# Kernel tuning notes

Hardware: AMD Instinct MI355X
Metric: run time of the kernel (lower is better)

The kernel has to match this reference:

```python
import jax, jax.numpy as jnp
import numpy as np
from functools import partial

H = 1024  # hidden_sz
B, T = 32, 256
NL = 4    # stacked LSTM layers
WSCALE = 0.02


def setup_inputs() -> dict:
    key = jax.random.key(0)
    ks = jax.random.split(key, 8)
    x = jax.random.normal(ks[0], (B, T, H), dtype=jnp.float32)
    h0 = jnp.zeros((B, H), dtype=jnp.float32)
    c0 = jnp.zeros((B, H), dtype=jnp.float32)
    # LSTM params per layer: kernel [H,4H], recurrent kernel [H,4H], bias [4H]
    Wk = jax.random.normal(ks[1], (NL, H, 4 * H), dtype=jnp.float32) * WSCALE
    Wr = jax.random.normal(ks[2], (NL, H, 4 * H), dtype=jnp.float32) * WSCALE
    b = jnp.zeros((NL, 4 * H), dtype=jnp.float32)
    # dense head
    Wd = jax.random.normal(ks[3], (H, H), dtype=jnp.float32) * WSCALE
    bd = jnp.zeros((H,), dtype=jnp.float32)
    return {"x": x, "h0": h0, "c0": c0, "Wk": Wk, "Wr": Wr, "b": b, "Wd": Wd, "bd": bd}


def _lstm_layer(x_tbd, h0, c0, Wk, Wr, b):
    # Keras LSTM with activation='relu', recurrent_activation='sigmoid'.
    # Gate order in keras kernels: i, f, c(candidate), o.
    xw = jnp.einsum('tbd,dg->tbg', x_tbd, Wk) + b  # precompute input projections [T,B,4H]

    def step(carry, xw_t):
        h, c = carry
        z = xw_t + h @ Wr  # [B,4H]
        i, f, g, o = jnp.split(z, 4, axis=-1)
        i = jax.nn.sigmoid(i)
        f = jax.nn.sigmoid(f)
        o = jax.nn.sigmoid(o)
        c = f * c + i * jax.nn.relu(g)
        h = o * jax.nn.relu(c)
        return (h, c), h

    (hT, cT), hs = jax.lax.scan(step, (h0, c0), xw)
    return hs, hT, cT  # hs: [T,B,H]


def reference(x, h0, c0, Wk, Wr, b, Wd, bd):
    # x: [B,T,H] -> time-major [T,B,H]
    seq = jnp.transpose(x, (1, 0, 2))
    h, c = h0, c0
    for l in range(NL):
        seq, h, c = _lstm_layer(seq, h, c, Wk[l], Wr[l], b[l])
        # dropout layers are identity at inference (training=False)
    out = jnp.einsum('tbh,hd->tbd', seq, Wd) + bd
    out = jnp.transpose(out, (1, 0, 2))  # back to [B,T,H]
    return out, h, c
```

## Files before the change

### kernel.cpp

```cpp
#include <hip/hip_runtime.h>

#define TT 256
#define BB 32
#define HH 1024
#define GG 4096

typedef __attribute__((ext_vector_type(8))) short short8;
typedef __attribute__((ext_vector_type(4))) float f32x4;

__device__ __forceinline__ unsigned short rne_bf16(float x) {
    unsigned u = __float_as_uint(x);
    unsigned r = (u + 0x7FFFu + ((u >> 16) & 1u)) >> 16;
    return (unsigned short)r;
}
__device__ __forceinline__ float bf16f(unsigned short s) {
    return __uint_as_float((unsigned)s << 16);
}

__global__ __launch_bounds__(256) void k_transpose3(const float* __restrict__ x,
                                                    unsigned short* __restrict__ s1,
                                                    unsigned short* __restrict__ s2,
                                                    unsigned short* __restrict__ s3) {
    int idx = blockIdx.x * 256 + threadIdx.x;
    int k4 = idx & 255;
    int tb = idx >> 8;
    int t = tb >> 5, b = tb & 31;
    float4 v = ((const float4*)x)[((size_t)b * TT + t) * 256 + k4];
    float xs[4] = {v.x, v.y, v.z, v.w};
    ushort4 o1, o2, o3;
    unsigned short* p1 = (unsigned short*)&o1;
    unsigned short* p2 = (unsigned short*)&o2;
    unsigned short* p3 = (unsigned short*)&o3;
#pragma unroll
    for (int e = 0; e < 4; ++e) {
        unsigned short q1 = rne_bf16(xs[e]);
        float r1 = xs[e] - bf16f(q1);
        unsigned short q2 = rne_bf16(r1);
        float r2 = r1 - bf16f(q2);
        p1[e] = q1; p2[e] = q2; p3[e] = rne_bf16(r2);
    }
    size_t off = (size_t)tb * HH + k4 * 4;
    *(ushort4*)&s1[off] = o1;
    *(ushort4*)&s2[off] = o2;
    *(ushort4*)&s3[off] = o3;
}

__global__ __launch_bounds__(256) void k_transpose(const float* __restrict__ x, float* __restrict__ seq) {
    int idx = blockIdx.x * 256 + threadIdx.x;
    int k4 = idx & 255;
    int tb = idx >> 8;
    int t = tb >> 5, b = tb & 31;
    float4 v = ((const float4*)x)[((size_t)b * TT + t) * 256 + k4];
    ((float4*)seq)[(size_t)tb * 256 + k4] = v;
}

__global__ __launch_bounds__(256) void k_init_hc(const float* __restrict__ h0, const float* __restrict__ c0,
                                                 float* __restrict__ h, float* __restrict__ c) {
    int i = blockIdx.x * 256 + threadIdx.x;
    ((float4*)h)[i] = ((const float4*)h0)[i];
    ((float4*)c)[i] = ((const float4*)c0)[i];
}

__global__ __launch_bounds__(256) void k_init_hc2(const float* __restrict__ h0, const float* __restrict__ c0,
                                                  float* __restrict__ h, float* __restrict__ c,
                                                  unsigned short* __restrict__ hb1,
                                                  unsigned short* __restrict__ hb2,
                                                  unsigned short* __restrict__ hb3) {
    int i = blockIdx.x * 256 + threadIdx.x;
    float4 hv = ((const float4*)h0)[i];
    ((float4*)h)[i] = hv;
    ((float4*)c)[i] = ((const float4*)c0)[i];
    float xs[4] = {hv.x, hv.y, hv.z, hv.w};
    ushort4 o1, o2, o3;
    unsigned short* p1 = (unsigned short*)&o1;
    unsigned short* p2 = (unsigned short*)&o2;
    unsigned short* p3 = (unsigned short*)&o3;
#pragma unroll
    for (int e = 0; e < 4; ++e) {
        unsigned short s1 = rne_bf16(xs[e]);
        float r1 = xs[e] - bf16f(s1);
        unsigned short s2 = rne_bf16(r1);
        float r2 = r1 - bf16f(s2);
        p1[e] = s1; p2[e] = s2; p3[e] = rne_bf16(r2);
    }
    *(ushort4*)&hb1[i * 4] = o1;
    *(ushort4*)&hb2[i * 4] = o2;
    *(ushort4*)&hb3[i * 4] = o3;
}

__global__ __launch_bounds__(256) void k_copy_hc(const float* __restrict__ h, const float* __restrict__ c,
                                                 float* __restrict__ oh, float* __restrict__ oc) {
    int i = blockIdx.x * 256 + threadIdx.x;
    ((float4*)oh)[i] = ((const float4*)h)[i];
    ((float4*)oc)[i] = ((const float4*)c)[i];
}

__global__ __launch_bounds__(256) void k_wrt(const float* __restrict__ Wr, float* __restrict__ WrT) {
    __shared__ float tile[64][65];
    int c0 = blockIdx.x * 64;
    int k0 = blockIdx.y * 64;
    int tid = threadIdx.x;
    int tr = tid >> 4, tc4 = tid & 15;
#pragma unroll
    for (int p = 0; p < 4; ++p) {
        int r = p * 16 + tr;
        float4 v = *(const float4*)&Wr[(size_t)(k0 + r) * GG + c0 + tc4 * 4];
        tile[r][tc4 * 4 + 0] = v.x;
        tile[r][tc4 * 4 + 1] = v.y;
        tile[r][tc4 * 4 + 2] = v.z;
        tile[r][tc4 * 4 + 3] = v.w;
    }
    __syncthreads();
#pragma unroll
    for (int p = 0; p < 4; ++p) {
        int cc = p * 16 + tr;
        float4 v;
        v.x = tile[tc4 * 4 + 0][cc];
        v.y = tile[tc4 * 4 + 1][cc];
        v.z = tile[tc4 * 4 + 2][cc];
        v.w = tile[tc4 * 4 + 3][cc];
        *(float4*)&WrT[(size_t)(c0 + cc) * 1024 + k0 + tc4 * 4] = v;
    }
}

__global__ __launch_bounds__(256) void k_wrt3(const float* __restrict__ Wr, unsigned short* __restrict__ W1,
                                              unsigned short* __restrict__ W2, unsigned short* __restrict__ W3) {
    __shared__ float tile[64][65];
    int c0 = blockIdx.x * 64;
    int k0 = blockIdx.y * 64;
    int tid = threadIdx.x;
    int tr = tid >> 4, tc4 = tid & 15;
#pragma unroll
    for (int p = 0; p < 4; ++p) {
        int r = p * 16 + tr;
        float4 v = *(const float4*)&Wr[(size_t)(k0 + r) * GG + c0 + tc4 * 4];
        tile[r][tc4 * 4 + 0] = v.x;
        tile[r][tc4 * 4 + 1] = v.y;
        tile[r][tc4 * 4 + 2] = v.z;
        tile[r][tc4 * 4 + 3] = v.w;
    }
    __syncthreads();
    int cc = tid & 63, kq = tid >> 6;
    int G = c0 + cc;
    int outrow = ((G & 1023) >> 2) * 16 + (G >> 10) * 4 + (G & 3);
    size_t obase = (size_t)outrow * 1024 + k0 + kq * 16;
    unsigned short t1[16], t2[16], t3[16];
#pragma unroll
    for (int e = 0; e < 16; ++e) {
        float v = tile[kq * 16 + e][cc];
        unsigned short s1 = rne_bf16(v);
        float r1 = v - bf16f(s1);
        unsigned short s2 = rne_bf16(r1);
        float r2 = r1 - bf16f(s2);
        t1[e] = s1; t2[e] = s2; t3[e] = rne_bf16(r2);
    }
#pragma unroll
    for (int hlf = 0; hlf < 2; ++hlf) {
        *(short8*)&W1[obase + hlf * 8] = *(short8*)&t1[hlf * 8];
        *(short8*)&W2[obase + hlf * 8] = *(short8*)&t2[hlf * 8];
        *(short8*)&W3[obase + hlf * 8] = *(short8*)&t3[hlf * 8];
    }
}

__global__ __launch_bounds__(256) void k_wt3(const float* __restrict__ W, int N,
                                             unsigned short* __restrict__ W1,
                                             unsigned short* __restrict__ W2,
                                             unsigned short* __restrict__ W3) {
    __shared__ float tile[64][65];
    int c0 = blockIdx.x * 64;
    int k0 = blockIdx.y * 64;
    int tid = threadIdx.x;
    int tr = tid >> 4, tc4 = tid & 15;
#pragma unroll
    for (int p = 0; p < 4; ++p) {
        int r = p * 16 + tr;
        float4 v = *(const float4*)&W[(size_t)(k0 + r) * N + c0 + tc4 * 4];
        tile[r][tc4 * 4 + 0] = v.x;
        tile[r][tc4 * 4 + 1] = v.y;
        tile[r][tc4 * 4 + 2] = v.z;
        tile[r][tc4 * 4 + 3] = v.w;
    }
    __syncthreads();
#pragma unroll
    for (int p = 0; p < 4; ++p) {
        int cc = p * 16 + tr;
        ushort4 o1, o2, o3;
        unsigned short* po1 = (unsigned short*)&o1;
        unsigned short* po2 = (unsigned short*)&o2;
        unsigned short* po3 = (unsigned short*)&o3;
#pragma unroll
        for (int e = 0; e < 4; ++e) {
            float v = tile[tc4 * 4 + e][cc];
            unsigned short s1 = rne_bf16(v);
            float r1 = v - bf16f(s1);
            unsigned short s2 = rne_bf16(r1);
            float r2 = r1 - bf16f(s2);
            po1[e] = s1; po2[e] = s2; po3[e] = rne_bf16(r2);
        }
        size_t off = (size_t)(c0 + cc) * 1024 + k0 + tc4 * 4;
        *(ushort4*)&W1[off] = o1;
        *(ushort4*)&W2[off] = o2;
        *(ushort4*)&W3[off] = o3;
    }
}

template <int MODE>
__global__ __launch_bounds__(256, 2) void k_gemm_mx3s(const unsigned short* __restrict__ A1,
                                                      const unsigned short* __restrict__ A2,
                                                      const unsigned short* __restrict__ A3,
                                                      const unsigned short* __restrict__ B1,
                                                      const unsigned short* __restrict__ B2,
                                                      const unsigned short* __restrict__ B3,
                                                      const float* __restrict__ bias, float* __restrict__ C) {
    __shared__ unsigned short Asl[3][6144];
    __shared__ unsigned short Bsl[3][6144];
    int tid = threadIdx.x;
    int m0 = blockIdx.x * 128, n0 = blockIdx.y * 128;
    int lane = tid & 63, wv = tid >> 6;
    int wr = (wv >> 1) * 64, wc = (wv & 1) * 64;
    int l15 = lane & 15, ko = (lane >> 4) * 8;

    f32x4 acc[4][4];
#pragma unroll
    for (int i = 0; i < 4; ++i)
#pragma unroll
        for (int j = 0; j < 4; ++j) acc[i][j] = (f32x4){0.f, 0.f, 0.f, 0.f};

    const unsigned short* Ag[3] = {A1, A2, A3};
    const unsigned short* Bg[3] = {B1, B2, B3};

    for (int k0 = 0; k0 < 1024; k0 += 32) {
#pragma unroll
        for (int sp = 0; sp < 3; ++sp) {
#pragma unroll
            for (int i = 0; i < 2; ++i) {
                int idx = i * 256 + tid;
                int r = idx >> 2, kq = idx & 3;
                short8 va = *(const short8*)&Ag[sp][(size_t)(m0 + r) * 1024 + k0 + kq * 8];
                *(short8*)&Asl[sp][r * 48 + kq * 8] = va;
                short8 vb = *(const short8*)&Bg[sp][(size_t)(n0 + r) * 1024 + k0 + kq * 8];
                *(short8*)&Bsl[sp][r * 48 + kq * 8] = vb;
            }
        }
        __syncthreads();

        short8 af[3][4];
#pragma unroll
        for (int mi = 0; mi < 4; ++mi) {
            int ro = (wr + mi * 16 + l15) * 48 + ko;
#pragma unroll
            for (int sp = 0; sp < 3; ++sp) af[sp][mi] = *(const short8*)&Asl[sp][ro];
        }
#pragma unroll
        for (int ni = 0; ni < 4; ++ni) {
            int co = (wc + ni * 16 + l15) * 48 + ko;
            short8 b0 = *(const short8*)&Bsl[0][co];
            short8 b1 = *(const short8*)&Bsl[1][co];
            short8 b2 = *(const short8*)&Bsl[2][co];
#pragma unroll
            for (int mi = 0; mi < 4; ++mi) {
                f32x4 a = acc[mi][ni];
                a = __builtin_amdgcn_mfma_f32_16x16x32_bf16(af[0][mi], b0, a, 0, 0, 0);
                a = __builtin_amdgcn_mfma_f32_16x16x32_bf16(af[1][mi], b0, a, 0, 0, 0);
                a = __builtin_amdgcn_mfma_f32_16x16x32_bf16(af[0][mi], b1, a, 0, 0, 0);
                a = __builtin_amdgcn_mfma_f32_16x16x32_bf16(af[2][mi], b0, a, 0, 0, 0);
                a = __builtin_amdgcn_mfma_f32_16x16x32_bf16(af[1][mi], b1, a, 0, 0, 0);
                a = __builtin_amdgcn_mfma_f32_16x16x32_bf16(af[0][mi], b2, a, 0, 0, 0);
                acc[mi][ni] = a;
            }
        }
        __syncthreads();
    }

#pragma unroll
    for (int ni = 0; ni < 4; ++ni) {
        int col = n0 + wc + ni * 16 + l15;
        float bv = bias[col];
#pragma unroll
        for (int mi = 0; mi < 4; ++mi) {
            int rbase = m0 + wr + mi * 16 + (lane >> 4) * 4;
#pragma unroll
            for (int r = 0; r < 4; ++r) {
                int m = rbase + r;
                if (MODE == 0) {
                    C[(size_t)m * 4096 + col] = acc[mi][ni][r] + bv;
                } else {
                    int t = m >> 5, b = m & 31;
                    C[((size_t)b * TT + t) * HH + col] = acc[mi][ni][r] + bv;
                }
            }
        }
    }
}

__global__ __launch_bounds__(256, 2) void k_gemm_mx3(const float* __restrict__ A,
                                                     const unsigned short* __restrict__ B1,
                                                     const unsigned short* __restrict__ B2,
                                                     const unsigned short* __restrict__ B3,
                                                     const float* __restrict__ bias, float* __restrict__ C) {
    __shared__ unsigned short Asl[3][6144];
    __shared__ unsigned short Bsl[3][6144];
    int tid = threadIdx.x;
    int m0 = blockIdx.x * 128, n0 = blockIdx.y * 128;
    int lane = tid & 63, wv = tid >> 6;
    int wr = (wv >> 1) * 64, wc = (wv & 1) * 64;
    int l15 = lane & 15, ko = (lane >> 4) * 8;

    f32x4 acc[4][4];
#pragma unroll
    for (int i = 0; i < 4; ++i)
#pragma unroll
        for (int j = 0; j < 4; ++j) acc[i][j] = (f32x4){0.f, 0.f, 0.f, 0.f};

    const unsigned short* Bg[3] = {B1, B2, B3};

    for (int k0 = 0; k0 < 1024; k0 += 32) {
#pragma unroll
        for (int i = 0; i < 4; ++i) {
            int idx = i * 256 + tid;
            int m = idx >> 3, kq = idx & 7;
            float4 v = *(const float4*)&A[(size_t)(m0 + m) * 1024 + k0 + kq * 4];
            float xs[4] = {v.x, v.y, v.z, v.w};
            ushort4 o1, o2, o3;
            unsigned short* po1 = (unsigned short*)&o1;
            unsigned short* po2 = (unsigned short*)&o2;
            unsigned short* po3 = (unsigned short*)&o3;
#pragma unroll
            for (int e = 0; e < 4; ++e) {
                unsigned short s1 = rne_bf16(xs[e]);
                float r1 = xs[e] - bf16f(s1);
                unsigned short s2 = rne_bf16(r1);
                float r2 = r1 - bf16f(s2);
                po1[e] = s1; po2[e] = s2; po3[e] = rne_bf16(r2);
            }
            int loff = m * 48 + kq * 4;
            *(ushort4*)&Asl[0][loff] = o1;
            *(ushort4*)&Asl[1][loff] = o2;
            *(ushort4*)&Asl[2][loff] = o3;
        }
#pragma unroll
        for (int sp = 0; sp < 3; ++sp) {
            const unsigned short* bg = Bg[sp];
#pragma unroll
            for (int i = 0; i < 2; ++i) {
                int idx = i * 256 + tid;
                int n = idx >> 2, kq = idx & 3;
                short8 v = *(const short8*)&bg[(size_t)(n0 + n) * 1024 + k0 + kq * 8];
                *(short8*)&Bsl[sp][n * 48 + kq * 8] = v;
            }
        }
        __syncthreads();

        short8 af[3][4];
#pragma unroll
        for (int mi = 0; mi < 4; ++mi) {
            int ro = (wr + mi * 16 + l15) * 48 + ko;
#pragma unroll
            for (int sp = 0; sp < 3; ++sp) af[sp][mi] = *(const short8*)&Asl[sp][ro];
        }
#pragma unroll
        for (int ni = 0; ni < 4; ++ni) {
            int co = (wc + ni * 16 + l15) * 48 + ko;
            short8 b0 = *(const short8*)&Bsl[0][co];
            short8 b1 = *(const short8*)&Bsl[1][co];
            short8 b2 = *(const short8*)&Bsl[2][co];
#pragma unroll
            for (int mi = 0; mi < 4; ++mi) {
                f32x4 a = acc[mi][ni];
                a = __builtin_amdgcn_mfma_f32_16x16x32_bf16(af[0][mi], b0, a, 0, 0, 0);
                a = __builtin_amdgcn_mfma_f32_16x16x32_bf16(af[1][mi], b0, a, 0, 0, 0);
                a = __builtin_amdgcn_mfma_f32_16x16x32_bf16(af[0][mi], b1, a, 0, 0, 0);
                a = __builtin_amdgcn_mfma_f32_16x16x32_bf16(af[2][mi], b0, a, 0, 0, 0);
                a = __builtin_amdgcn_mfma_f32_16x16x32_bf16(af[1][mi], b1, a, 0, 0, 0);
                a = __builtin_amdgcn_mfma_f32_16x16x32_bf16(af[0][mi], b2, a, 0, 0, 0);
                acc[mi][ni] = a;
            }
        }
        __syncthreads();
    }

#pragma unroll
    for (int ni = 0; ni < 4; ++ni) {
        int col = n0 + wc + ni * 16 + l15;
        float bv = bias[col];
#pragma unroll
        for (int mi = 0; mi < 4; ++mi) {
            int rbase = m0 + wr + mi * 16 + (lane >> 4) * 4;
#pragma unroll
            for (int r = 0; r < 4; ++r)
                C[(size_t)(rbase + r) * 4096 + col] = acc[mi][ni][r] + bv;
        }
    }
}

template <int MODE>
__global__ __launch_bounds__(256) void k_gemm(const float* __restrict__ A, const float* __restrict__ W,
                                              const float* __restrict__ bias, float* __restrict__ C, int N) {
    __shared__ float As[16][132];
    __shared__ float Bs[16][132];
    const int K = 1024;
    int tid = threadIdx.x;
    int m0 = blockIdx.x * 128, n0 = blockIdx.y * 128;
    int tx = tid & 15, ty = tid >> 4;
    int a_row = tid >> 2, a_kq = tid & 3;
    int b_cq = tid & 31, b_k = tid >> 5;
    float acc[8][8];
#pragma unroll
    for (int i = 0; i < 8; ++i)
#pragma unroll
        for (int jj = 0; jj < 8; ++jj) acc[i][jj] = 0.f;

    for (int kc = 0; kc < K; kc += 16) {
#pragma unroll
        for (int it = 0; it < 2; ++it) {
            int row = a_row + it * 64;
            float4 v = *(const float4*)&A[(size_t)(m0 + row) * K + kc + a_kq * 4];
            As[a_kq * 4 + 0][row] = v.x;
            As[a_kq * 4 + 1][row] = v.y;
            As[a_kq * 4 + 2][row] = v.z;
            As[a_kq * 4 + 3][row] = v.w;
        }
#pragma unroll
        for (int it = 0; it < 2; ++it) {
            int kk = b_k + it * 8;
            float4 v = *(const float4*)&W[(size_t)(kc + kk) * N + n0 + b_cq * 4];
            *(float4*)&Bs[kk][b_cq * 4] = v;
        }
        __syncthreads();
#pragma unroll
        for (int kk = 0; kk < 16; ++kk) {
            float4 a0 = *(const float4*)&As[kk][ty * 8];
            float4 a1 = *(const float4*)&As[kk][ty * 8 + 4];
            float4 b0 = *(const float4*)&Bs[kk][tx * 8];
            float4 b1 = *(const float4*)&Bs[kk][tx * 8 + 4];
            float am[8] = {a0.x, a0.y, a0.z, a0.w, a1.x, a1.y, a1.z, a1.w};
            float bv[8] = {b0.x, b0.y, b0.z, b0.w, b1.x, b1.y, b1.z, b1.w};
#pragma unroll
            for (int i = 0; i < 8; ++i)
#pragma unroll
                for (int jj = 0; jj < 8; ++jj) acc[i][jj] += am[i] * bv[jj];
        }
        __syncthreads();
    }
#pragma unroll
    for (int i = 0; i < 8; ++i) {
        int m = m0 + ty * 8 + i;
#pragma unroll
        for (int jj = 0; jj < 8; jj += 4) {
            int n = n0 + tx * 8 + jj;
            float4 v;
            v.x = acc[i][jj + 0] + bias[n + 0];
            v.y = acc[i][jj + 1] + bias[n + 1];
            v.z = acc[i][jj + 2] + bias[n + 2];
            v.w = acc[i][jj + 3] + bias[n + 3];
            if (MODE == 0) {
                *(float4*)&C[(size_t)m * N + n] = v;
            } else {
                int t = m >> 5, b = m & 31;
                *(float4*)&C[((size_t)b * TT + t) * HH + n] = v;
            }
        }
    }
}

__global__ __launch_bounds__(512) void k_step_mfma(
    const unsigned short* __restrict__ Wb1, const unsigned short* __restrict__ Wb2,
    const unsigned short* __restrict__ Wb3,
    const unsigned short* __restrict__ Ha1, const unsigned short* __restrict__ Ha2,
    const unsigned short* __restrict__ Ha3,
    unsigned short* __restrict__ Ho1, unsigned short* __restrict__ Ho2,
    unsigned short* __restrict__ Ho3,
    const float* __restrict__ xw_t,
    unsigned short* __restrict__ sq1, unsigned short* __restrict__ sq2,
    unsigned short* __restrict__ sq3, float* __restrict__ seq_t,
    float* __restrict__ h_out, float* __restrict__ c) {
    __shared__ float zs[8][16][33];
    int tid = threadIdx.x;
    int lane = tid & 63, wv = tid >> 6;
    int blk = blockIdx.x;
    int l15 = lane & 15, ko = (lane >> 4) * 8;

    int rb = tid >> 2, rd = tid & 3;
    float pz[4];
    if (tid < 128) {
#pragma unroll
        for (int g = 0; g < 4; ++g) pz[g] = xw_t[rb * GG + g * HH + blk * 4 + rd];
    }

    size_t bbase  = ((size_t)blk * 16 + l15) * 1024 + ko;
    size_t abase0 = (size_t)l15 * 1024 + ko;
    size_t abase1 = (size_t)(16 + l15) * 1024 + ko;

    f32x4 acc0 = (f32x4){0.f, 0.f, 0.f, 0.f};
    f32x4 acc1 = (f32x4){0.f, 0.f, 0.f, 0.f};

#pragma unroll
    for (int kt = 0; kt < 4; ++kt) {
        int kk = (wv * 4 + kt) * 32;
        short8 b0  = *(const short8*)&Wb1[bbase + kk];
        short8 b1  = *(const short8*)&Wb2[bbase + kk];
        short8 b2  = *(const short8*)&Wb3[bbase + kk];
        short8 a00 = *(const short8*)&Ha1[abase0 + kk];
        short8 a01 = *(const short8*)&Ha2[abase0 + kk];
        short8 a02 = *(const short8*)&Ha3[abase0 + kk];
        short8 a10 = *(const short8*)&Ha1[abase1 + kk];
        short8 a11 = *(const short8*)&Ha2[abase1 + kk];
        short8 a12 = *(const short8*)&Ha3[abase1 + kk];
        acc0 = __builtin_amdgcn_mfma_f32_16x16x32_bf16(a00, b0, acc0, 0, 0, 0);
        acc0 = __builtin_amdgcn_mfma_f32_16x16x32_bf16(a01, b0, acc0, 0, 0, 0);
        acc0 = __builtin_amdgcn_mfma_f32_16x16x32_bf16(a00, b1, acc0, 0, 0, 0);
        acc0 = __builtin_amdgcn_mfma_f32_16x16x32_bf16(a02, b0, acc0, 0, 0, 0);
        acc0 = __builtin_amdgcn_mfma_f32_16x16x32_bf16(a01, b1, acc0, 0, 0, 0);
        acc0 = __builtin_amdgcn_mfma_f32_16x16x32_bf16(a00, b2, acc0, 0, 0, 0);
        acc1 = __builtin_amdgcn_mfma_f32_16x16x32_bf16(a10, b0, acc1, 0, 0, 0);
        acc1 = __builtin_amdgcn_mfma_f32_16x16x32_bf16(a11, b0, acc1, 0, 0, 0);
        acc1 = __builtin_amdgcn_mfma_f32_16x16x32_bf16(a10, b1, acc1, 0, 0, 0);
        acc1 = __builtin_amdgcn_mfma_f32_16x16x32_bf16(a12, b0, acc1, 0, 0, 0);
        acc1 = __builtin_amdgcn_mfma_f32_16x16x32_bf16(a11, b1, acc1, 0, 0, 0);
        acc1 = __builtin_amdgcn_mfma_f32_16x16x32_bf16(a10, b2, acc1, 0, 0, 0);
    }

#pragma unroll
    for (int r = 0; r < 4; ++r) {
        zs[wv][l15][(lane >> 4) * 4 + r]      = acc0[r];
        zs[wv][l15][16 + (lane >> 4) * 4 + r] = acc1[r];
    }
    __syncthreads();

    if (tid < 128) {
        float zz[4];
#pragma unroll
        for (int g = 0; g < 4; ++g) {
            float s = pz[g];
#pragma unroll
            for (int u = 0; u < 8; ++u) s += zs[u][g * 4 + rd][rb];
            zz[g] = s;
        }
        float si = 1.f / (1.f + expf(-zz[0]));
        float sf = 1.f / (1.f + expf(-zz[1]));
        float gg = fmaxf(zz[2], 0.f);
        float so = 1.f / (1.f + expf(-zz[3]));
        int hi = rb * HH + blk * 4 + rd;
        float cv = c[hi];
        cv = sf * cv + si * gg;
        c[hi] = cv;
        float hn = so * fmaxf(cv, 0.f);
        h_out[hi] = hn;
        unsigned short s1 = rne_bf16(hn);
        float r1 = hn - bf16f(s1);
        unsigned short s2 = rne_bf16(r1);
        float r2 = r1 - bf16f(s2);
        unsigned short s3 = rne_bf16(r2);
        Ho1[hi] = s1; Ho2[hi] = s2; Ho3[hi] = s3;
        if (sq1) {
            sq1[hi] = s1; sq2[hi] = s2; sq3[hi] = s3;
        } else {
            seq_t[hi] = hn;
        }
    }
}

__global__ __launch_bounds__(512) void k_step_T3(const float* __restrict__ WrT, const float* __restrict__ xw_t,
                                                 float* __restrict__ seq_t, const float* __restrict__ h_in,
                                                 float* __restrict__ h_out, float* __restrict__ c) {
    __shared__ float h_lds[34816];
    __shared__ float zred[8][32][17];
    int tid = threadIdx.x;
    int j = tid & 15, ks = tid >> 4;
    int hc0 = blockIdx.x * 4;
    int col = (j >> 2) * HH + hc0 + (j & 3);

    const float4* WrT4 = (const float4*)WrT;
    int wbase = col * 256 + ks * 8;
    float4 w[8];
#pragma unroll
    for (int q = 0; q < 8; ++q) w[q] = WrT4[wbase + q];

    int rb = tid >> 2, rd = tid & 3;
    float pz[4];
    if (tid < 128) {
#pragma unroll
        for (int g = 0; g < 4; ++g) pz[g] = xw_t[rb * GG + g * HH + hc0 + rd];
    }

    const float4* hp4 = (const float4*)h_in;
    float4* hl4w = (float4*)h_lds;
#pragma unroll 8
    for (int it = 0; it < 16; ++it) {
        int gi = it * 512 + tid;
        float4 v = hp4[gi];
        int b = gi >> 8, kk = gi & 255;
        hl4w[b * 272 + (kk >> 4) * 17 + (kk & 15)] = v;
    }
    __syncthreads();

    const float4* hl4 = (const float4*)h_lds;
    int base4 = (ks >> 1) * 17 + (ks & 1) * 8;
    float acc[32];
#pragma unroll
    for (int b = 0; b < 32; ++b) acc[b] = 0.f;
#pragma unroll
    for (int q = 0; q < 8; ++q) {
        float4 wq = w[q];
#pragma unroll
        for (int b = 0; b < 32; ++b) {
            float4 hv = hl4[b * 272 + base4 + q];
            acc[b] += wq.x * hv.x + wq.y * hv.y + wq.z * hv.z + wq.w * hv.w;
        }
    }
#pragma unroll
    for (int b = 0; b < 32; ++b) {
        acc[b] += __shfl_xor(acc[b], 16);
        acc[b] += __shfl_xor(acc[b], 32);
    }
    int wv = tid >> 6;
    if ((ks & 3) == 0) {
#pragma unroll
        for (int b = 0; b < 32; ++b) zred[wv][b][j] = acc[b];
    }
    __syncthreads();

    if (tid < 128) {
        float zz[4];
#pragma unroll
        for (int g = 0; g < 4; ++g) {
            float s = pz[g];
#pragma unroll
            for (int u = 0; u < 8; ++u) s += zred[u][rb][g * 4 + rd];
            zz[g] = s;
        }
        float si = 1.f / (1.f + expf(-zz[0]));
        float sf = 1.f / (1.f + expf(-zz[1]));
        float gg = fmaxf(zz[2], 0.f);
        float so = 1.f / (1.f + expf(-zz[3]));
        float cv = c[rb * HH + hc0 + rd];
        cv = sf * cv + si * gg;
        c[rb * HH + hc0 + rd] = cv;
        float hn = so * fmaxf(cv, 0.f);
        h_out[rb * HH + hc0 + rd] = hn;
        seq_t[rb * HH + hc0 + rd] = hn;
    }
}

__global__ __launch_bounds__(256) void k_step(const float* __restrict__ Wr, const float* __restrict__ xw_t,
                                              float* __restrict__ seq_t, const float* __restrict__ h_in,
                                              float* __restrict__ h_out, float* __restrict__ c) {
    __shared__ float zred[4][32][17];
    int tid = threadIdx.x;
    int j = tid & 15, ks = tid >> 4;
    int hc0 = blockIdx.x * 4;
    int col = (j >> 2) * HH + hc0 + (j & 3);
    float4 w[16];
#pragma unroll
    for (int q = 0; q < 16; ++q) {
        size_t kb = (size_t)(ks * 64 + q * 4) * GG + col;
        w[q].x = Wr[kb];
        w[q].y = Wr[kb + GG];
        w[q].z = Wr[kb + 2 * (size_t)GG];
        w[q].w = Wr[kb + 3 * (size_t)GG];
    }
    const float4* hp = (const float4*)h_in;
    int kq0 = ks * 16;
    float acc[32];
#pragma unroll
    for (int b = 0; b < 32; ++b) acc[b] = 0.f;
#pragma unroll
    for (int q = 0; q < 16; ++q) {
        float4 wq = w[q];
#pragma unroll
        for (int b = 0; b < 32; ++b) {
            float4 hv = hp[b * 256 + kq0 + q];
            acc[b] += wq.x * hv.x + wq.y * hv.y + wq.z * hv.z + wq.w * hv.w;
        }
    }
#pragma unroll
    for (int b = 0; b < 32; ++b) {
        acc[b] += __shfl_xor(acc[b], 16);
        acc[b] += __shfl_xor(acc[b], 32);
    }
    int wv = tid >> 6;
    if ((ks & 3) == 0) {
#pragma unroll
        for (int b = 0; b < 32; ++b) zred[wv][b][j] = acc[b];
    }
    __syncthreads();
    if (tid < 128) {
        int rb = tid >> 2, rd = tid & 3;
        float zz[4];
#pragma unroll
        for (int g = 0; g < 4; ++g) {
            float s = xw_t[rb * GG + g * HH + hc0 + rd];
#pragma unroll
            for (int u = 0; u < 4; ++u) s += zred[u][rb][g * 4 + rd];
            zz[g] = s;
        }
        float si = 1.f / (1.f + expf(-zz[0]));
        float sf = 1.f / (1.f + expf(-zz[1]));
        float gg = fmaxf(zz[2], 0.f);
        float so = 1.f / (1.f + expf(-zz[3]));
        float cv = c[rb * HH + hc0 + rd];
        cv = sf * cv + si * gg;
        c[rb * HH + hc0 + rd] = cv;
        float hn = so * fmaxf(cv, 0.f);
        h_out[rb * HH + hc0 + rd] = hn;
        seq_t[rb * HH + hc0 + rd] = hn;
    }
}

extern "C" void kernel_launch(void* const* d_in, const int* in_sizes, int n_in,
                              void* d_out, int out_size, void* d_ws, size_t ws_size,
                              hipStream_t stream) {
    const float* x  = (const float*)d_in[0];
    const float* h0 = (const float*)d_in[1];
    const float* c0 = (const float*)d_in[2];
    const float* Wk = (const float*)d_in[3];
    const float* Wr = (const float*)d_in[4];
    const float* bs = (const float*)d_in[5];
    const float* Wd = (const float*)d_in[6];
    const float* bd = (const float*)d_in[7];
    float* out = (float*)d_out;
    float* ws  = (float*)d_ws;

    float* xw  = ws;
    float* seq = ws + 33554432;
    float* h0b = seq + 8388608;
    float* h1b = h0b + 32768;
    float* c   = h1b + 32768;
    float* wrt = c + 32768;
    const size_t base_floats = 46235648;
    unsigned short* wkt1 = (unsigned short*)(ws + base_floats);
    unsigned short* wkt2 = wkt1 + 4194304;
    unsigned short* wkt3 = wkt2 + 4194304;
    unsigned short* wrb1 = wkt3 + 4194304;
    unsigned short* wrb2 = wrb1 + 4194304;
    unsigned short* wrb3 = wrb2 + 4194304;
    unsigned short* hA1  = wrb3 + 4194304;
    unsigned short* hA2  = hA1 + 32768;
    unsigned short* hA3  = hA2 + 32768;
    unsigned short* hB1  = hA3 + 32768;
    unsigned short* hB2  = hB1 + 32768;
    unsigned short* hB3  = hB2 + 32768;
    unsigned short* sq1  = (unsigned short*)seq;
    unsigned short* sq2  = sq1 + 8388608;
    unsigned short* sq3  = hB3 + 32768;

    const size_t mfma2_floats = base_floats + ((size_t)6 * 4194304 * 2 + 6 * 32768 * 2 + 3) / 4;
    const size_t mfma3_floats = mfma2_floats + ((size_t)8388608 * 2 + 3) / 4;
    bool fast     = ws_size >= base_floats * 4;
    bool mfma_ok  = ws_size >= (base_floats + (size_t)3 * 4194304 / 2 * 4) ;
    bool mfma2_ok = ws_size >= mfma2_floats * 4;
    bool mfma3_ok = ws_size >= mfma3_floats * 4;
    mfma_ok = ws_size >= base_floats * 4 + (size_t)3 * 4194304 * 2;

    if (mfma3_ok) {
        k_transpose3<<<8192, 256, 0, stream>>>(x, sq1, sq2, sq3);
        k_init_hc2<<<32, 256, 0, stream>>>(h0, c0, h0b, c, hA1, hA2, hA3);
    } else {
        k_transpose<<<8192, 256, 0, stream>>>(x, seq);
        if (mfma2_ok)
            k_init_hc2<<<32, 256, 0, stream>>>(h0, c0, h0b, c, hA1, hA2, hA3);
        else
            k_init_hc<<<32, 256, 0, stream>>>(h0, c0, h0b, c);
    }

    for (int l = 0; l < 4; ++l) {
        const float* Wrl = Wr + (size_t)l * 1024 * 4096;
        const float* Wkl = Wk + (size_t)l * 1024 * 4096;
        if (mfma3_ok) {
            k_wt3<<<dim3(64, 16), 256, 0, stream>>>(Wkl, 4096, wkt1, wkt2, wkt3);
            k_gemm_mx3s<0><<<dim3(64, 32), 256, 0, stream>>>(sq1, sq2, sq3, wkt1, wkt2, wkt3,
                                                             bs + l * 4096, xw);
        } else if (mfma_ok) {
            k_wt3<<<dim3(64, 16), 256, 0, stream>>>(Wkl, 4096, wkt1, wkt2, wkt3);
            k_gemm_mx3<<<dim3(64, 32), 256, 0, stream>>>(seq, wkt1, wkt2, wkt3, bs + l * 4096, xw);
        } else {
            k_gemm<0><<<dim3(64, 32), 256, 0, stream>>>(seq, Wkl, bs + l * 4096, xw, 4096);
        }
        if (mfma2_ok) {
            k_wrt3<<<dim3(64, 16), 256, 0, stream>>>(Wrl, wrb1, wrb2, wrb3);
            for (int t = 0; t < TT; ++t) {
                float* hout = (t & 1) ? h0b : h1b;
                const unsigned short* i1 = (t & 1) ? hB1 : hA1;
                const unsigned short* i2 = (t & 1) ? hB2 : hA2;
                const unsigned short* i3 = (t & 1) ? hB3 : hA3;
                unsigned short* o1 = (t & 1) ? hA1 : hB1;
                unsigned short* o2 = (t & 1) ? hA2 : hB2;
                unsigned short* o3 = (t & 1) ? hA3 : hB3;
                if (mfma3_ok)
                    k_step_mfma<<<256, 512, 0, stream>>>(wrb1, wrb2, wrb3, i1, i2, i3, o1, o2, o3,
                                                         xw + (size_t)t * (BB * GG),
                                                         sq1 + (size_t)t * (BB * HH),
                                                         sq2 + (size_t)t * (BB * HH),
                                                         sq3 + (size_t)t * (BB * HH),
                                                         nullptr, hout, c);
                else
                    k_step_mfma<<<256, 512, 0, stream>>>(wrb1, wrb2, wrb3, i1, i2, i3, o1, o2, o3,
                                                         xw + (size_t)t * (BB * GG),
                                                         nullptr, nullptr, nullptr,
                                                         seq + (size_t)t * (BB * HH), hout, c);
            }
        } else {
            if (fast) k_wrt<<<dim3(64, 16), 256, 0, stream>>>(Wrl, wrt);
            for (int t = 0; t < TT; ++t) {
                const float* hin = (t & 1) ? h1b : h0b;
                float* hout      = (t & 1) ? h0b : h1b;
                if (fast)
                    k_step_T3<<<256, 512, 0, stream>>>(wrt, xw + (size_t)t * (BB * GG),
                                                       seq + (size_t)t * (BB * HH), hin, hout, c);
                else
                    k_step<<<256, 256, 0, stream>>>(Wrl, xw + (size_t)t * (BB * GG),
                                                    seq + (size_t)t * (BB * HH), hin, hout, c);
            }
        }
    }

    if (mfma3_ok) {
        k_wt3<<<dim3(16, 16), 256, 0, stream>>>(Wd, 1024, wkt1, wkt2, wkt3);
        k_gemm_mx3s<1><<<dim3(64, 8), 256, 0, stream>>>(sq1, sq2, sq3, wkt1, wkt2, wkt3, bd, out);
    } else {
        k_gemm<1><<<dim3(64, 8), 256, 0, stream>>>(seq, Wd, bd, out, 1024);
    }
    k_copy_hc<<<32, 256, 0, stream>>>(h0b, c, out + 8388608, out + 8388608 + 32768);
}
```

Before: 13.54 ms.

## Register-prefetch GEMM tiles and widen recurrent step to 8 hidden units per block

The split-bf16 GEMM now loads the next K-slice of A and B into registers while the current slice is being computed, so global load latency overlaps the MFMA work. The per-timestep recurrent kernel now has each block handle two 16-row weight column groups, covering 8 hidden units, and reuses the loaded h fragments across both. This halves the grid to 128 blocks and doubles the per-block work. The trade-off is fewer blocks per step on a 256-CU device, which may underfill the GPU, along with higher register pressure in the GEMM.

```diff
diff --git a/kernel.cpp b/kernel.cpp
--- a/kernel.cpp
+++ b/kernel.cpp
@@ -228,21 +228,38 @@
 
     const unsigned short* Ag[3] = {A1, A2, A3};
     const unsigned short* Bg[3] = {B1, B2, B3};
+    int srow = tid >> 2, skq = tid & 3;
+
+    short8 ra[3][2], rbv[3][2];
+#pragma unroll
+    for (int sp = 0; sp < 3; ++sp)
+#pragma unroll
+        for (int i = 0; i < 2; ++i) {
+            int r = srow + i * 64;
+            ra[sp][i]  = *(const short8*)&Ag[sp][(size_t)(m0 + r) * 1024 + skq * 8];
+            rbv[sp][i] = *(const short8*)&Bg[sp][(size_t)(n0 + r) * 1024 + skq * 8];
+        }
 
     for (int k0 = 0; k0 < 1024; k0 += 32) {
 #pragma unroll
-        for (int sp = 0; sp < 3; ++sp) {
+        for (int sp = 0; sp < 3; ++sp)
 #pragma unroll
             for (int i = 0; i < 2; ++i) {
-                int idx = i * 256 + tid;
-                int r = idx >> 2, kq = idx & 3;
-                short8 va = *(const short8*)&Ag[sp][(size_t)(m0 + r) * 1024 + k0 + kq * 8];
-                *(short8*)&Asl[sp][r * 48 + kq * 8] = va;
-                short8 vb = *(const short8*)&Bg[sp][(size_t)(n0 + r) * 1024 + k0 + kq * 8];
-                *(short8*)&Bsl[sp][r * 48 + kq * 8] = vb;
+                int r = srow + i * 64;
+                *(short8*)&Asl[sp][r * 48 + skq * 8] = ra[sp][i];
+                *(short8*)&Bsl[sp][r * 48 + skq * 8] = rbv[sp][i];
             }
-        }
         __syncthreads();
+        if (k0 + 32 < 1024) {
+#pragma unroll
+            for (int sp = 0; sp < 3; ++sp)
+#pragma unroll
+                for (int i = 0; i < 2; ++i) {
+                    int r = srow + i * 64;
+                    ra[sp][i]  = *(const short8*)&Ag[sp][(size_t)(m0 + r) * 1024 + k0 + 32 + skq * 8];
+                    rbv[sp][i] = *(const short8*)&Bg[sp][(size_t)(n0 + r) * 1024 + k0 + 32 + skq * 8];
+                }
+        }
 
         short8 af[3][4];
 #pragma unroll
@@ -463,7 +480,7 @@
     }
 }
 
-__global__ __launch_bounds__(512) void k_step_mfma(
+__global__ __launch_bounds__(512) void k_step_mfma8(
     const unsigned short* __restrict__ Wb1, const unsigned short* __restrict__ Wb2,
     const unsigned short* __restrict__ Wb3,
     const unsigned short* __restrict__ Ha1, const unsigned short* __restrict__ Ha2,
@@ -474,73 +491,86 @@
     unsigned short* __restrict__ sq1, unsigned short* __restrict__ sq2,
     unsigned short* __restrict__ sq3, float* __restrict__ seq_t,
     float* __restrict__ h_out, float* __restrict__ c) {
-    __shared__ float zs[8][16][33];
+    __shared__ float zs[8][2][16][33];
     int tid = threadIdx.x;
     int lane = tid & 63, wv = tid >> 6;
-    int blk = blockIdx.x;
+    int nb = blockIdx.x;
     int l15 = lane & 15, ko = (lane >> 4) * 8;
 
-    int rb = tid >> 2, rd = tid & 3;
+    int rb = tid >> 3, e8 = tid & 7;
     float pz[4];
-    if (tid < 128) {
-#pragma unroll
-        for (int g = 0; g < 4; ++g) pz[g] = xw_t[rb * GG + g * HH + blk * 4 + rd];
-    }
-
-    size_t bbase  = ((size_t)blk * 16 + l15) * 1024 + ko;
+    if (tid < 256) {
+#pragma unroll
+        for (int g = 0; g < 4; ++g) pz[g] = xw_t[rb * GG + g * HH + nb * 8 + e8];
+    }
+
     size_t abase0 = (size_t)l15 * 1024 + ko;
     size_t abase1 = (size_t)(16 + l15) * 1024 + ko;
 
-    f32x4 acc0 = (f32x4){0.f, 0.f, 0.f, 0.f};
-    f32x4 acc1 = (f32x4){0.f, 0.f, 0.f, 0.f};
+    f32x4 acc[2][2];
+#pragma unroll
+    for (int i = 0; i < 2; ++i)
+#pragma unroll
+        for (int j = 0; j < 2; ++j) acc[i][j] = (f32x4){0.f, 0.f, 0.f, 0.f};
 
 #pragma unroll
     for (int kt = 0; kt < 4; ++kt) {
         int kk = (wv * 4 + kt) * 32;
-        short8 b0  = *(const short8*)&Wb1[bbase + kk];
-        short8 b1  = *(const short8*)&Wb2[bbase + kk];
-        short8 b2  = *(const short8*)&Wb3[bbase + kk];
         short8 a00 = *(const short8*)&Ha1[abase0 + kk];
         short8 a01 = *(const short8*)&Ha2[abase0 + kk];
         short8 a02 = *(const short8*)&Ha3[abase0 + kk];
         short8 a10 = *(const short8*)&Ha1[abase1 + kk];
         short8 a11 = *(const short8*)&Ha2[abase1 + kk];
         short8 a12 = *(const short8*)&Ha3[abase1 + kk];
-        acc0 = __builtin_amdgcn_mfma_f32_16x16x32_bf16(a00, b0, acc0, 0, 0, 0);
-        acc0 = __builtin_amdgcn_mfma_f32_16x16x32_bf16(a01, b0, acc0, 0, 0, 0);
-        acc0 = __builtin_amdgcn_mfma_f32_16x16x32_bf16(a00, b1, acc0, 0, 0, 0);
-        acc0 = __builtin_amdgcn_mfma_f32_16x16x32_bf16(a02, b0, acc0, 0, 0, 0);
-        acc0 = __builtin_amdgcn_mfma_f32_16x16x32_bf16(a01, b1, acc0, 0, 0, 0);
-        acc0 = __builtin_amdgcn_mfma_f32_16x16x32_bf16(a00, b2, acc0, 0, 0, 0);
-        acc1 = __builtin_amdgcn_mfma_f32_16x16x32_bf16(a10, b0, acc1, 0, 0, 0);
-        acc1 = __builtin_amdgcn_mfma_f32_16x16x32_bf16(a11, b0, acc1, 0, 0, 0);
-        acc1 = __builtin_amdgcn_mfma_f32_16x16x32_bf16(a10, b1, acc1, 0, 0, 0);
-        acc1 = __builtin_amdgcn_mfma_f32_16x16x32_bf16(a12, b0, acc1, 0, 0, 0);
-        acc1 = __builtin_amdgcn_mfma_f32_16x16x32_bf16(a11, b1, acc1, 0, 0, 0);
-        acc1 = __builtin_amdgcn_mfma_f32_16x16x32_bf16(a10, b2, acc1, 0, 0, 0);
-    }
-
-#pragma unroll
-    for (int r = 0; r < 4; ++r) {
-        zs[wv][l15][(lane >> 4) * 4 + r]      = acc0[r];
-        zs[wv][l15][16 + (lane >> 4) * 4 + r] = acc1[r];
-    }
+#pragma unroll
+        for (int cg = 0; cg < 2; ++cg) {
+            size_t bbase = ((size_t)(nb * 2 + cg) * 16 + l15) * 1024 + ko;
+            short8 b0 = *(const short8*)&Wb1[bbase + kk];
+            short8 b1 = *(const short8*)&Wb2[bbase + kk];
+            short8 b2 = *(const short8*)&Wb3[bbase + kk];
+            f32x4 a0 = acc[cg][0];
+            a0 = __builtin_amdgcn_mfma_f32_16x16x32_bf16(a00, b0, a0, 0, 0, 0);
+            a0 = __builtin_amdgcn_mfma_f32_16x16x32_bf16(a01, b0, a0, 0, 0, 0);
+            a0 = __builtin_amdgcn_mfma_f32_16x16x32_bf16(a00, b1, a0, 0, 0, 0);
+            a0 = __builtin_amdgcn_mfma_f32_16x16x32_bf16(a02, b0, a0, 0, 0, 0);
+            a0 = __builtin_amdgcn_mfma_f32_16x16x32_bf16(a01, b1, a0, 0, 0, 0);
+            a0 = __builtin_amdgcn_mfma_f32_16x16x32_bf16(a00, b2, a0, 0, 0, 0);
+            acc[cg][0] = a0;
+            f32x4 a1 = acc[cg][1];
+            a1 = __builtin_amdgcn_mfma_f32_16x16x32_bf16(a10, b0, a1, 0, 0, 0);
+            a1 = __builtin_amdgcn_mfma_f32_16x16x32_bf16(a11, b0, a1, 0, 0, 0);
+            a1 = __builtin_amdgcn_mfma_f32_16x16x32_bf16(a10, b1, a1, 0, 0, 0);
+            a1 = __builtin_amdgcn_mfma_f32_16x16x32_bf16(a12, b0, a1, 0, 0, 0);
+            a1 = __builtin_amdgcn_mfma_f32_16x16x32_bf16(a11, b1, a1, 0, 0, 0);
+            a1 = __builtin_amdgcn_mfma_f32_16x16x32_bf16(a10, b2, a1, 0, 0, 0);
+            acc[cg][1] = a1;
+        }
+    }
+
+#pragma unroll
+    for (int cg = 0; cg < 2; ++cg)
+#pragma unroll
+        for (int r = 0; r < 4; ++r) {
+            zs[wv][cg][l15][(lane >> 4) * 4 + r]      = acc[cg][0][r];
+            zs[wv][cg][l15][16 + (lane >> 4) * 4 + r] = acc[cg][1][r];
+        }
     __syncthreads();
 
-    if (tid < 128) {
+    if (tid < 256) {
+        int cg = e8 >> 2, d = e8 & 3;
         float zz[4];
 #pragma unroll
         for (int g = 0; g < 4; ++g) {
             float s = pz[g];
 #pragma unroll
-            for (int u = 0; u < 8; ++u) s += zs[u][g * 4 + rd][rb];
+            for (int u = 0; u < 8; ++u) s += zs[u][cg][g * 4 + d][rb];
             zz[g] = s;
         }
         float si = 1.f / (1.f + expf(-zz[0]));
         float sf = 1.f / (1.f + expf(-zz[1]));
         float gg = fmaxf(zz[2], 0.f);
         float so = 1.f / (1.f + expf(-zz[3]));
-        int hi = rb * HH + blk * 4 + rd;
+        int hi = rb * HH + nb * 8 + e8;
         float cv = c[hi];
         cv = sf * cv + si * gg;
         c[hi] = cv;
@@ -747,10 +777,9 @@
     const size_t mfma2_floats = base_floats + ((size_t)6 * 4194304 * 2 + 6 * 32768 * 2 + 3) / 4;
     const size_t mfma3_floats = mfma2_floats + ((size_t)8388608 * 2 + 3) / 4;
     bool fast     = ws_size >= base_floats * 4;
-    bool mfma_ok  = ws_size >= (base_floats + (size_t)3 * 4194304 / 2 * 4) ;
+    bool mfma_ok  = ws_size >= base_floats * 4 + (size_t)3 * 4194304 * 2;
     bool mfma2_ok = ws_size >= mfma2_floats * 4;
     bool mfma3_ok = ws_size >= mfma3_floats * 4;
-    mfma_ok = ws_size >= base_floats * 4 + (size_t)3 * 4194304 * 2;
 
     if (mfma3_ok) {
         k_transpose3<<<8192, 256, 0, stream>>>(x, sq1, sq2, sq3);
@@ -787,17 +816,17 @@
                 unsigned short* o2 = (t & 1) ? hA2 : hB2;
                 unsigned short* o3 = (t & 1) ? hA3 : hB3;
                 if (mfma3_ok)
-                    k_step_mfma<<<256, 512, 0, stream>>>(wrb1, wrb2, wrb3, i1, i2, i3, o1, o2, o3,
-                                                         xw + (size_t)t * (BB * GG),
-                                                         sq1 + (size_t)t * (BB * HH),
-                                                         sq2 + (size_t)t * (BB * HH),
-                                                         sq3 + (size_t)t * (BB * HH),
-                                                         nullptr, hout, c);
+                    k_step_mfma8<<<128, 512, 0, stream>>>(wrb1, wrb2, wrb3, i1, i2, i3, o1, o2, o3,
+                                                          xw + (size_t)t * (BB * GG),
+                                                          sq1 + (size_t)t * (BB * HH),
+                                                          sq2 + (size_t)t * (BB * HH),
+                                                          sq3 + (size_t)t * (BB * HH),
+                                                          nullptr, hout, c);
                 else
-                    k_step_mfma<<<256, 512, 0, stream>>>(wrb1, wrb2, wrb3, i1, i2, i3, o1, o2, o3,
-                                                         xw + (size_t)t * (BB * GG),
-                                                         nullptr, nullptr, nullptr,
-                                                         seq + (size_t)t * (BB * HH), hout, c);
+                    k_step_mfma8<<<128, 512, 0, stream>>>(wrb1, wrb2, wrb3, i1, i2, i3, o1, o2, o3,
+                                                          xw + (size_t)t * (BB * GG),
+                                                          nullptr, nullptr, nullptr,
+                                                          seq + (size_t)t * (BB * HH), hout, c);
             }
         } else {
             if (fast) k_wrt<<<dim3(64, 16), 256, 0, stream>>>(Wrl, wrt);
```

New measurement: 15.91 ms. 1.18x slower.
